# Performance work log

Measured on AMD Instinct MI355X. Metric: run time of the kernel, lower is better.

The kernel has to match this reference:

```python
import jax, jax.numpy as jnp
import numpy as np

EPS = 1e-5
TEMP = 2.0

def _dwconv(x, k, dil):
    # depthwise conv, NCHW, kernel OIHW with I=1, groups=C, 'same' padding
    p = dil
    return jax.lax.conv_general_dilated(
        x, k, window_strides=(1, 1), padding=[(p, p), (p, p)],
        rhs_dilation=(dil, dil),
        dimension_numbers=('NCHW', 'OIHW', 'NCHW'),
        feature_group_count=x.shape[1])

def _bn_gelu(y, g, b, m, v):
    scale = (g / jnp.sqrt(v + EPS))[None, :, None, None]
    z = (y - m[None, :, None, None]) * scale + b[None, :, None, None]
    return jax.nn.gelu(z, approximate=False)  # torch nn.GELU default = exact erf

def _pw(feat, w, b):
    # 1x1 pointwise conv with bias
    return jnp.einsum('oi,bihw->bohw', w, feat) + b[None, :, None, None]

def _forward(x, rw, rb,
             e0_k, e0_g, e0_b, e0_m, e0_v, e0_pw, e0_pb,
             e1_k, e1_g, e1_b, e1_m, e1_v, e1_pw, e1_pb,
             e2_k, e2_g, e2_b, e2_m, e2_v, e2_pw, e2_pb):
    # ---- global routing (eval mode: no noise) ----
    pooled = x.mean(axis=(2, 3))                    # [B, C]
    logits = pooled @ rw.T + rb                     # [B, 3]
    prob = jax.nn.softmax(logits / TEMP, axis=-1)
    tp, ti = jax.lax.top_k(prob, 1)                 # top_k = 1
    w = (tp / tp.sum(axis=-1, keepdims=True))[:, 0] # [B], == 1.0 for k=1
    idx = ti[:, 0]                                  # [B]

    # ---- heterogeneous experts, each over full batch, masked by weight ----
    f0 = _pw(_bn_gelu(_dwconv(x, e0_k, 1), e0_g, e0_b, e0_m, e0_v), e0_pw, e0_pb)
    f1 = _pw(_bn_gelu(_dwconv(x, e1_k, 2), e1_g, e1_b, e1_m, e1_v), e1_pw, e1_pb)
    f2 = _pw(_bn_gelu(jnp.einsum('oi,bihw->bohw', e2_k, x), e2_g, e2_b, e2_m, e2_v), e2_pw, e2_pb)

    out = jnp.zeros_like(x)
    for i, fi in enumerate((f0, f1, f2)):
        wi = jnp.where(idx == i, w, 0.0)[:, None, None, None]
        out = out + wi * fi
    return out

def setup_inputs() -> dict:
    key = jax.random.key(0)
    ks = jax.random.split(key, 24)
    B, C, H, W = 32, 256, 64, 64
    d = {
        'x': jax.random.normal(ks[0], (B, C, H, W), jnp.float32),
        'rw': jax.random.normal(ks[1], (3, C), jnp.float32) * 0.02,
        'rb': jnp.zeros((3,), jnp.float32),
    }
    kshapes = [(C, 1, 3, 3), (C, 1, 3, 3), (C, C)]
    for i in range(3):
        base = 2 + i * 4
        d[f'e{i}_k'] = jax.random.normal(ks[base], kshapes[i], jnp.float32) * 0.1
        d[f'e{i}_g'] = jnp.ones((C,), jnp.float32)
        d[f'e{i}_b'] = jnp.zeros((C,), jnp.float32)
        d[f'e{i}_m'] = jax.random.normal(ks[base + 1], (C,), jnp.float32) * 0.1
        d[f'e{i}_v'] = jax.random.uniform(ks[base + 2], (C,), jnp.float32, 0.5, 1.5)
        d[f'e{i}_pw'] = jax.random.normal(ks[base + 3], (C, C), jnp.float32) / np.sqrt(C)
        d[f'e{i}_pb'] = jnp.zeros((C,), jnp.float32)
    return d

def reference(x, rw, rb,
              e0_k, e0_g, e0_b, e0_m, e0_v, e0_pw, e0_pb,
              e1_k, e1_g, e1_b, e1_m, e1_v, e1_pw, e1_pb,
              e2_k, e2_g, e2_b, e2_m, e2_v, e2_pw, e2_pb):
    return _forward(x, rw, rb,
                    e0_k, e0_g, e0_b, e0_m, e0_v, e0_pw, e0_pb,
                    e1_k, e1_g, e1_b, e1_m, e1_v, e1_pw, e1_pb,
                    e2_k, e2_g, e2_b, e2_m, e2_v, e2_pw, e2_pb)
```

## Files before the change

kernel.cpp:

```cpp
#include <hip/hip_runtime.h>
#include <math.h>

#define C 256
#define H 64
#define W 64
#define B 32
#define HW (H*W)
#define EPS 1e-5f
#define LSTR 72
#define LSTR2 64

typedef __attribute__((ext_vector_type(8))) short short8;
typedef __attribute__((ext_vector_type(4))) short short4v;
typedef __attribute__((ext_vector_type(4))) float f32x4;

__device__ __forceinline__ float gelu_exact(float z) {
    return 0.5f * z * (1.0f + erff(z * 0.70710678f));
}
__device__ __forceinline__ short f2bf(float f) {
    union { float f; unsigned u; } v; v.f = f;
    unsigned r = v.u + 0x7fffu + ((v.u >> 16) & 1u);
    return (short)(r >> 16);
}
__device__ __forceinline__ float bf2f(short s) {
    union { unsigned u; float f; } v; v.u = ((unsigned)(unsigned short)s) << 16;
    return v.f;
}

__global__ __launch_bounds__(256) void pool_kernel(const float* __restrict__ x,
                                                   float* __restrict__ pooled) {
    int bc = blockIdx.x;
    const float4* p4 = (const float4*)(x + (size_t)bc * HW);
    int t = threadIdx.x;
    float s = 0.f;
    for (int i = t; i < HW/4; i += 256) {
        float4 v = p4[i];
        s += v.x + v.y + v.z + v.w;
    }
    for (int off = 32; off > 0; off >>= 1) s += __shfl_down(s, off, 64);
    __shared__ float wsum[4];
    if ((t & 63) == 0) wsum[t >> 6] = s;
    __syncthreads();
    if (t == 0) pooled[bc] = (wsum[0]+wsum[1]+wsum[2]+wsum[3]) * (1.f/HW);
}

__global__ void route_kernel(const float* __restrict__ pooled,
                             const float* __restrict__ rw,
                             const float* __restrict__ rb,
                             int* __restrict__ idx) {
    int b = blockIdx.x;
    int t = threadIdx.x;
    int e = t >> 6, lane = t & 63;
    const float* p = pooled + b*C;
    const float* w = rw + e*C;
    float s = 0.f;
#pragma unroll
    for (int i = 0; i < 4; ++i) s += p[lane + i*64] * w[lane + i*64];
    for (int off = 32; off > 0; off >>= 1) s += __shfl_down(s, off, 64);
    __shared__ float lg[3];
    if (lane == 0) lg[e] = s + rb[e];
    __syncthreads();
    if (t == 0) {
        int best = 0; float bv = lg[0];
        if (lg[1] > bv) { bv = lg[1]; best = 1; }
        if (lg[2] > bv) { bv = lg[2]; best = 2; }
        idx[b] = best;
    }
}

__global__ __launch_bounds__(256) void prep_kernel(
    const float* __restrict__ s0, const float* __restrict__ s1,
    const float* __restrict__ s2, const float* __restrict__ s3,
    const float* __restrict__ e0k, const float* __restrict__ e1k,
    const float* __restrict__ g0, const float* __restrict__ b0,
    const float* __restrict__ m0, const float* __restrict__ v0,
    const float* __restrict__ g1, const float* __restrict__ b1,
    const float* __restrict__ m1, const float* __restrict__ v1,
    const float* __restrict__ g2, const float* __restrict__ b2,
    const float* __restrict__ m2, const float* __restrict__ v2,
    short* __restrict__ apackAll, float* __restrict__ kf0, float* __restrict__ kf1,
    float* __restrict__ scAll, float* __restrict__ shAll)
{
    if (blockIdx.x < 192) {
        int gid = blockIdx.x * 256 + threadIdx.x;
        int mat = gid >> 13;
        int c   = gid & 8191;
        int lane = c & 63;
        int ktmt = c >> 6;
        int mt = ktmt & 15, kt = ktmt >> 4;
        int o  = mt*16 + (lane & 15);
        int ci = kt*32 + (lane >> 4)*8;
        const float* src = (mat == 0) ? s0 : (mat == 1) ? s1 :
                           (mat == 2 || mat == 4) ? s2 : s3;
        bool lo = (mat >= 4);
        const float* p = src + o*C + ci;
        short8 v;
#pragma unroll
        for (int j = 0; j < 8; ++j) {
            float f = p[j];
            short hj = f2bf(f);
            v[j] = lo ? f2bf(f - bf2f(hj)) : hj;
        }
        *(short8*)&apackAll[(size_t)gid * 8] = v;
    } else {
        int t = threadIdx.x;
        {
            float s = g0[t] / sqrtf(v0[t] + EPS);
            scAll[t] = s; shAll[t] = b0[t] - m0[t]*s;
#pragma unroll
            for (int j = 0; j < 9; ++j) kf0[t*12+j] = e0k[t*9+j]*s;
            kf0[t*12+9] = 0.f; kf0[t*12+10] = 0.f; kf0[t*12+11] = 0.f;
        }
        {
            float s = g1[t] / sqrtf(v1[t] + EPS);
            scAll[C+t] = s; shAll[C+t] = b1[t] - m1[t]*s;
#pragma unroll
            for (int j = 0; j < 9; ++j) kf1[t*12+j] = e1k[t*9+j]*s;
            kf1[t*12+9] = 0.f; kf1[t*12+10] = 0.f; kf1[t*12+11] = 0.f;
        }
        {
            float s = g2[t] / sqrtf(v2[t] + EPS);
            scAll[2*C+t] = s; shAll[2*C+t] = b2[t] - m2[t]*s;
        }
    }
}

template<int DIL>
__device__ __forceinline__ void conv_rows(const float* __restrict__ x,
                                          const float* __restrict__ kf,
                                          const float* __restrict__ sh,
                                          short* __restrict__ lds,
                                          int b, int h, int t) {
    const int strip = t & 7;
    const int w0 = strip * 8;
    const int cib = t >> 3;
#pragma unroll 1
    for (int iter = 0; iter < 8; ++iter) {
        int ci = iter*32 + cib;
        const float* xpl = x + (size_t)(b*C + ci) * HW;
        float fr[3][16];
        bool rv[3];
#pragma unroll
        for (int ky = 0; ky < 3; ++ky) {
            int y = h + (ky - 1)*DIL;
            rv[ky] = ((unsigned)y < H);
            if (rv[ky]) {
                const float* row = xpl + y*W;
                float4 fa = (strip > 0) ? *(const float4*)(row + w0 - 4) : float4{0,0,0,0};
                float4 fb = *(const float4*)(row + w0);
                float4 fc = *(const float4*)(row + w0 + 4);
                float4 fd = (strip < 7) ? *(const float4*)(row + w0 + 8) : float4{0,0,0,0};
                fr[ky][0]=fa.x; fr[ky][1]=fa.y; fr[ky][2]=fa.z; fr[ky][3]=fa.w;
                fr[ky][4]=fb.x; fr[ky][5]=fb.y; fr[ky][6]=fb.z; fr[ky][7]=fb.w;
                fr[ky][8]=fc.x; fr[ky][9]=fc.y; fr[ky][10]=fc.z; fr[ky][11]=fc.w;
                fr[ky][12]=fd.x; fr[ky][13]=fd.y; fr[ky][14]=fd.z; fr[ky][15]=fd.w;
            }
        }
        float4 k0 = *(const float4*)(kf + ci*12);
        float4 k1v = *(const float4*)(kf + ci*12 + 4);
        float wk[9] = {k0.x,k0.y,k0.z,k0.w,k1v.x,k1v.y,k1v.z,k1v.w, kf[ci*12+8]};
        float acc8[8] = {0,0,0,0,0,0,0,0};
#pragma unroll
        for (int ky = 0; ky < 3; ++ky) {
            if (rv[ky]) {
#pragma unroll
                for (int kx = 0; kx < 3; ++kx) {
                    float wv = wk[ky*3+kx];
                    const int base = 4 + (kx - 1)*DIL;
#pragma unroll
                    for (int j = 0; j < 8; ++j) acc8[j] += wv * fr[ky][base + j];
                }
            }
        }
        float shv = sh[ci];
        int w0s = w0 ^ ((((unsigned)ci >> 3) & 3) << 4);
        short8 res;
#pragma unroll
        for (int j = 0; j < 8; ++j) res[j] = f2bf(gelu_exact(acc8[j] + shv));
        *(short8*)&lds[ci*LSTR + w0s] = res;
    }
}

__global__ __launch_bounds__(256) void k1_feat(
    const float* __restrict__ x, const int* __restrict__ idx,
    const float* __restrict__ kf0, const float* __restrict__ kf1,
    const float* __restrict__ scAll, const float* __restrict__ shAll,
    short* __restrict__ featfrag)
{
    __shared__ short lds[C*LSTR];
    const int h = blockIdx.x, b = blockIdx.y;
    const int t = threadIdx.x;
    const int lane = t & 63, wid = t >> 6;
    const int l15 = lane & 15, quad = lane >> 4;
    const int e = idx[b];
    if (e >= 2) return;

    if (e == 0) conv_rows<1>(x, kf0, shAll,     lds, b, h, t);
    else        conv_rows<2>(x, kf1, shAll + C, lds, b, h, t);
    __syncthreads();
#pragma unroll
    for (int itr = 0; itr < 8; ++itr) {
        int chunk = itr*4 + wid;
        int kt = chunk & 7, pt = chunk >> 3;
        int wv = pt*16 + l15;
        int cb = kt*32 + quad*8;
        short8 v;
#pragma unroll
        for (int r = 0; r < 8; ++r) {
            int ci = cb + r;
            v[r] = lds[ci*LSTR + (wv ^ ((((unsigned)ci >> 3) & 3) << 4))];
        }
        *(short8*)&featfrag[(((size_t)(b*C + h*4 + pt)*8 + kt)*64 + lane)*8] = v;
    }
}

__device__ __forceinline__ void gemm3(const short* __restrict__ aH,
                                      const short* __restrict__ aL,
                                      const short* __restrict__ ldsA,
                                      const short* __restrict__ ldsB,
                                      int lane, int wid, f32x4 acc[4][4])
{
    const int l15 = lane & 15, quad = lane >> 4;
    for (int kt = 0; kt < 8; ++kt) {
        int cb = kt*32 + quad*8;
        short8 bH[4], bL[4];
#pragma unroll
        for (int wt = 0; wt < 4; ++wt) {
            int wv = (wt*16 + l15) ^ (quad << 4);
            short8 vH, vL;
#pragma unroll
            for (int r = 0; r < 8; ++r) {
                vH[r] = ldsA[(cb + r)*LSTR2 + wv];
                vL[r] = ldsB[(cb + r)*LSTR2 + wv];
            }
            bH[wt] = vH; bL[wt] = vL;
        }
        short8 fH[4], fL[4];
#pragma unroll
        for (int i = 0; i < 4; ++i) {
            size_t off = ((size_t)(kt*16 + wid*4 + i)*64 + lane)*8;
            fH[i] = *(const short8*)&aH[off];
            fL[i] = *(const short8*)&aL[off];
        }
#pragma unroll
        for (int i = 0; i < 4; ++i)
#pragma unroll
            for (int wt = 0; wt < 4; ++wt) {
                acc[i][wt] = __builtin_amdgcn_mfma_f32_16x16x32_bf16(fH[i], bH[wt], acc[i][wt], 0, 0, 0);
                acc[i][wt] = __builtin_amdgcn_mfma_f32_16x16x32_bf16(fH[i], bL[wt], acc[i][wt], 0, 0, 0);
                acc[i][wt] = __builtin_amdgcn_mfma_f32_16x16x32_bf16(fL[i], bH[wt], acc[i][wt], 0, 0, 0);
            }
    }
}

__global__ __launch_bounds__(256) void k1e2(
    const float* __restrict__ x, const int* __restrict__ idx,
    const float* __restrict__ scAll, const float* __restrict__ shAll,
    const short* __restrict__ apackAll, const float* __restrict__ e2pb,
    float* __restrict__ out)
{
    __shared__ short ldsA[C*LSTR2];
    __shared__ short ldsB[C*LSTR2];
    const int h = blockIdx.x, b = blockIdx.y;
    const int t = threadIdx.x;
    const int lane = t & 63, wid = t >> 6;
    const int l15 = lane & 15, quad = lane >> 4;
    if (idx[b] != 2) return;

    {
        const int strip = t & 7, w0 = strip*8, cib = t >> 3;
#pragma unroll 1
        for (int iter = 0; iter < 8; ++iter) {
            int ci = iter*32 + cib;
            const float* row = x + ((size_t)(b*C + ci)*H + h)*W;
            float4 fa = *(const float4*)(row + w0);
            float4 fb = *(const float4*)(row + w0 + 4);
            float f[8] = {fa.x,fa.y,fa.z,fa.w,fb.x,fb.y,fb.z,fb.w};
            short8 hi, lo;
#pragma unroll
            for (int j = 0; j < 8; ++j) {
                short hj = f2bf(f[j]);
                hi[j] = hj;
                lo[j] = f2bf(f[j] - bf2f(hj));
            }
            int w0s = w0 ^ ((((unsigned)ci >> 3) & 3) << 4);
            *(short8*)&ldsA[ci*LSTR2 + w0s] = hi;
            *(short8*)&ldsB[ci*LSTR2 + w0s] = lo;
        }
    }
    __syncthreads();

    f32x4 acc[4][4];
#pragma unroll
    for (int i = 0; i < 4; ++i)
#pragma unroll
        for (int wt = 0; wt < 4; ++wt) acc[i][wt] = (f32x4){0.f,0.f,0.f,0.f};
    gemm3(apackAll + (size_t)3*65536, apackAll + (size_t)5*65536,
          ldsA, ldsB, lane, wid, acc);
    __syncthreads();

    {
        const float* sc2 = scAll + 2*C;
        const float* sh2 = shAll + 2*C;
#pragma unroll
        for (int i = 0; i < 4; ++i) {
            int cob = wid*64 + i*16 + quad*4;
            float4 s4 = *(const float4*)&sc2[cob];
            float4 h4 = *(const float4*)&sh2[cob];
            float ss[4] = {s4.x, s4.y, s4.z, s4.w};
            float hh[4] = {h4.x, h4.y, h4.z, h4.w};
#pragma unroll
            for (int r = 0; r < 4; ++r) {
                int co = cob + r;
                int sw = ((co >> 3) & 3) << 4;
#pragma unroll
                for (int wt = 0; wt < 4; ++wt) {
                    float f = gelu_exact(acc[i][wt][r]*ss[r] + hh[r]);
                    short hj = f2bf(f);
                    short lj = f2bf(f - bf2f(hj));
                    int a = co*LSTR2 + ((wt*16 + l15) ^ sw);
                    ldsA[a] = hj; ldsB[a] = lj;
                }
            }
        }
    }
    __syncthreads();

#pragma unroll
    for (int i = 0; i < 4; ++i)
#pragma unroll
        for (int wt = 0; wt < 4; ++wt) acc[i][wt] = (f32x4){0.f,0.f,0.f,0.f};
    gemm3(apackAll + (size_t)2*65536, apackAll + (size_t)4*65536,
          ldsA, ldsB, lane, wid, acc);

#pragma unroll
    for (int i = 0; i < 4; ++i) {
        int ob = wid*64 + i*16 + quad*4;
        float4 p4 = *(const float4*)&e2pb[ob];
        float pbv[4] = {p4.x, p4.y, p4.z, p4.w};
#pragma unroll
        for (int wt = 0; wt < 4; ++wt) {
            int w = wt*16 + l15;
#pragma unroll
            for (int r = 0; r < 4; ++r) {
                out[((size_t)(b*C + ob + r))*HW + h*W + w] = acc[i][wt][r] + pbv[r];
            }
        }
    }
}

__global__ __launch_bounds__(256) void k2b_out(
    const int* __restrict__ idx, const short* __restrict__ featfrag,
    const short* __restrict__ apackAll,
    const float* __restrict__ e0pb, const float* __restrict__ e1pb,
    float* __restrict__ out)
{
    const int pblk = blockIdx.x;
    const int oblk = blockIdx.y;
    const int b = blockIdx.z;
    const int t = threadIdx.x, lane = t & 63, wid = t >> 6;
    const int l15 = lane & 15, quad = lane >> 4;
    const int e = idx[b];
    if (e >= 2) return;
    const short* pwf = apackAll + (size_t)e * 65536;
    const float* pb = (e == 0) ? e0pb : e1pb;

    f32x4 acc[2][8];
#pragma unroll
    for (int a = 0; a < 2; ++a)
#pragma unroll
        for (int i = 0; i < 8; ++i) acc[a][i] = (f32x4){0.f,0.f,0.f,0.f};

    const short* fbase = featfrag + ((size_t)(b*C + pblk*8 + wid*2)*8)*512;
    for (int kt = 0; kt < 8; ++kt) {
        short8 af[2];
#pragma unroll
        for (int a = 0; a < 2; ++a)
            af[a] = *(const short8*)&fbase[((size_t)(a*8 + kt)*64 + lane)*8];
        short8 bf[8];
#pragma unroll
        for (int i = 0; i < 8; ++i)
            bf[i] = *(const short8*)&pwf[((size_t)(kt*16 + oblk*8 + i)*64 + lane)*8];
#pragma unroll
        for (int a = 0; a < 2; ++a)
#pragma unroll
            for (int i = 0; i < 8; ++i)
                acc[a][i] = __builtin_amdgcn_mfma_f32_16x16x32_bf16(
                    af[a], bf[i], acc[a][i], 0, 0, 0);
    }

#pragma unroll
    for (int i = 0; i < 8; ++i) {
        int o = oblk*128 + i*16 + l15;
        float pbv = pb[o];
#pragma unroll
        for (int a = 0; a < 2; ++a) {
            int p = pblk*128 + wid*32 + a*16 + quad*4;
            f32x4 v = acc[a][i];
            float4 sv = {v[0]+pbv, v[1]+pbv, v[2]+pbv, v[3]+pbv};
            *(float4*)(out + (size_t)(b*C + o)*HW + p) = sv;
        }
    }
}

extern "C" void kernel_launch(void* const* d_in, const int* in_sizes, int n_in,
                              void* d_out, int out_size, void* d_ws, size_t ws_size,
                              hipStream_t stream) {
    const float* x    = (const float*)d_in[0];
    const float* rw   = (const float*)d_in[1];
    const float* rb   = (const float*)d_in[2];
    const float* e0k  = (const float*)d_in[3];
    const float* e0g  = (const float*)d_in[4];
    const float* e0b  = (const float*)d_in[5];
    const float* e0m  = (const float*)d_in[6];
    const float* e0v  = (const float*)d_in[7];
    const float* e0pw = (const float*)d_in[8];
    const float* e0pb = (const float*)d_in[9];
    const float* e1k  = (const float*)d_in[10];
    const float* e1g  = (const float*)d_in[11];
    const float* e1b  = (const float*)d_in[12];
    const float* e1m  = (const float*)d_in[13];
    const float* e1v  = (const float*)d_in[14];
    const float* e1pw = (const float*)d_in[15];
    const float* e1pb = (const float*)d_in[16];
    const float* e2k  = (const float*)d_in[17];
    const float* e2g  = (const float*)d_in[18];
    const float* e2b  = (const float*)d_in[19];
    const float* e2m  = (const float*)d_in[20];
    const float* e2v  = (const float*)d_in[21];
    const float* e2pw = (const float*)d_in[22];
    const float* e2pb = (const float*)d_in[23];
    float* out = (float*)d_out;

    char* wsb = (char*)d_ws;
    float* pooled   = (float*)wsb;
    int*   idx      = (int*)(wsb + 32768);
    float* scAll    = (float*)(wsb + 32896);
    float* shAll    = (float*)(wsb + 35968);
    float* kf0      = (float*)(wsb + 39040);
    float* kf1      = (float*)(wsb + 51328);
    short* apackAll = (short*)(wsb + 63616);
    short* featfrag = (short*)(wsb + (1u << 20));

    pool_kernel<<<B*C, 256, 0, stream>>>(x, pooled);
    route_kernel<<<B, 192, 0, stream>>>(pooled, rw, rb, idx);
    prep_kernel<<<193, 256, 0, stream>>>(e0pw, e1pw, e2pw, e2k, e0k, e1k,
                                         e0g, e0b, e0m, e0v,
                                         e1g, e1b, e1m, e1v,
                                         e2g, e2b, e2m, e2v,
                                         apackAll, kf0, kf1, scAll, shAll);
    k1_feat<<<dim3(H, B), 256, 0, stream>>>(x, idx, kf0, kf1, scAll, shAll,
                                            featfrag);
    k1e2<<<dim3(H, B), 256, 0, stream>>>(x, idx, scAll, shAll, apackAll,
                                         e2pb, out);
    k2b_out<<<dim3(32, 2, B), 256, 0, stream>>>(idx, featfrag, apackAll,
                                                e0pb, e1pb, out);
}
```

Measured before the change: 424.3 us.

## Fuse depthwise conv and pointwise GEMM into one kernel with transposed LDS layout

```diff
diff --git a/kernel.cpp b/kernel.cpp
--- a/kernel.cpp
+++ b/kernel.cpp
@@ -7,8 +7,7 @@
 #define B 32
 #define HW (H*W)
 #define EPS 1e-5f
-#define LSTR 72
-#define LSTR2 64
+#define LSTR2 256
 
 typedef __attribute__((ext_vector_type(8))) short short8;
 typedef __attribute__((ext_vector_type(4))) short short4v;
@@ -25,6 +24,16 @@
 __device__ __forceinline__ float bf2f(short s) {
     union { unsigned u; float f; } v; v.u = ((unsigned)(unsigned short)s) << 16;
     return v.f;
+}
+__device__ __forceinline__ int swz8(int w) {
+    return (((w & 7) ^ ((w >> 3) & 7)) << 3);
+}
+__device__ __forceinline__ void swz_hb(int bx, int by, int& h, int& b) {
+    int wg  = bx + (by << 6);
+    int xcd = wg & 7, lin = wg >> 3;
+    b = lin >> 3;
+    int j = lin & 7;
+    h = (((xcd + b) & 7) << 3) + j;
 }
 
 __global__ __launch_bounds__(256) void pool_kernel(const float* __restrict__ x,
@@ -42,30 +51,6 @@
     if ((t & 63) == 0) wsum[t >> 6] = s;
     __syncthreads();
     if (t == 0) pooled[bc] = (wsum[0]+wsum[1]+wsum[2]+wsum[3]) * (1.f/HW);
-}
-
-__global__ void route_kernel(const float* __restrict__ pooled,
-                             const float* __restrict__ rw,
-                             const float* __restrict__ rb,
-                             int* __restrict__ idx) {
-    int b = blockIdx.x;
-    int t = threadIdx.x;
-    int e = t >> 6, lane = t & 63;
-    const float* p = pooled + b*C;
-    const float* w = rw + e*C;
-    float s = 0.f;
-#pragma unroll
-    for (int i = 0; i < 4; ++i) s += p[lane + i*64] * w[lane + i*64];
-    for (int off = 32; off > 0; off >>= 1) s += __shfl_down(s, off, 64);
-    __shared__ float lg[3];
-    if (lane == 0) lg[e] = s + rb[e];
-    __syncthreads();
-    if (t == 0) {
-        int best = 0; float bv = lg[0];
-        if (lg[1] > bv) { bv = lg[1]; best = 1; }
-        if (lg[2] > bv) { bv = lg[2]; best = 2; }
-        idx[b] = best;
-    }
 }
 
 __global__ __launch_bounds__(256) void prep_kernel(
@@ -78,6 +63,8 @@
     const float* __restrict__ m1, const float* __restrict__ v1,
     const float* __restrict__ g2, const float* __restrict__ b2,
     const float* __restrict__ m2, const float* __restrict__ v2,
+    const float* __restrict__ pooled, const float* __restrict__ rw,
+    const float* __restrict__ rb, int* __restrict__ idx,
     short* __restrict__ apackAll, float* __restrict__ kf0, float* __restrict__ kf1,
     float* __restrict__ scAll, float* __restrict__ shAll)
 {
@@ -102,7 +89,7 @@
             v[j] = lo ? f2bf(f - bf2f(hj)) : hj;
         }
         *(short8*)&apackAll[(size_t)gid * 8] = v;
-    } else {
+    } else if (blockIdx.x == 192) {
         int t = threadIdx.x;
         {
             float s = g0[t] / sqrtf(v0[t] + EPS);
@@ -122,15 +109,40 @@
             float s = g2[t] / sqrtf(v2[t] + EPS);
             scAll[2*C+t] = s; shAll[2*C+t] = b2[t] - m2[t]*s;
         }
+    } else {
+        int t = threadIdx.x;
+        if (t < 192) {
+            int e = t >> 6, lane = t & 63;
+            __shared__ float lg[3*B];
+            for (int b = 0; b < B; ++b) {
+                const float* p = pooled + b*C;
+                const float* w = rw + e*C;
+                float s = 0.f;
+#pragma unroll
+                for (int i = 0; i < 4; ++i) s += p[lane + i*64] * w[lane + i*64];
+                for (int off = 32; off > 0; off >>= 1) s += __shfl_down(s, off, 64);
+                if (lane == 0) lg[b*3 + e] = s + rb[e];
+            }
+            __syncthreads();
+            if (t < B) {
+                float l0 = lg[t*3], l1 = lg[t*3+1], l2 = lg[t*3+2];
+                int best = 0; float bv = l0;
+                if (l1 > bv) { bv = l1; best = 1; }
+                if (l2 > bv) { bv = l2; best = 2; }
+                idx[t] = best;
+            }
+        } else {
+            __syncthreads();
+        }
     }
 }
 
 template<int DIL>
-__device__ __forceinline__ void conv_rows(const float* __restrict__ x,
-                                          const float* __restrict__ kf,
-                                          const float* __restrict__ sh,
-                                          short* __restrict__ lds,
-                                          int b, int h, int t) {
+__device__ __forceinline__ void conv_rows_t(const float* __restrict__ x,
+                                            const float* __restrict__ kf,
+                                            const float* __restrict__ sh,
+                                            short* __restrict__ lds,
+                                            int b, int h, int t) {
     const int strip = t & 7;
     const int w0 = strip * 8;
     const int cib = t >> 3;
@@ -173,67 +185,90 @@
             }
         }
         float shv = sh[ci];
-        int w0s = w0 ^ ((((unsigned)ci >> 3) & 3) << 4);
-        short8 res;
-#pragma unroll
-        for (int j = 0; j < 8; ++j) res[j] = f2bf(gelu_exact(acc8[j] + shv));
-        *(short8*)&lds[ci*LSTR + w0s] = res;
-    }
-}
-
-__global__ __launch_bounds__(256) void k1_feat(
+#pragma unroll
+        for (int j = 0; j < 8; ++j) {
+            int w = w0 + j;
+            lds[w*LSTR2 + (ci ^ swz8(w))] = f2bf(gelu_exact(acc8[j] + shv));
+        }
+    }
+}
+
+__global__ __launch_bounds__(256) void kconv(
     const float* __restrict__ x, const int* __restrict__ idx,
     const float* __restrict__ kf0, const float* __restrict__ kf1,
-    const float* __restrict__ scAll, const float* __restrict__ shAll,
-    short* __restrict__ featfrag)
+    const float* __restrict__ shAll, const short* __restrict__ apackAll,
+    const float* __restrict__ e0pb, const float* __restrict__ e1pb,
+    float* __restrict__ out)
 {
-    __shared__ short lds[C*LSTR];
-    const int h = blockIdx.x, b = blockIdx.y;
+    __shared__ short lds[W*LSTR2];
+    int h, b;
+    swz_hb(blockIdx.x, blockIdx.y, h, b);
+    const int e = idx[b];
+    if (e >= 2) return;
     const int t = threadIdx.x;
     const int lane = t & 63, wid = t >> 6;
     const int l15 = lane & 15, quad = lane >> 4;
-    const int e = idx[b];
-    if (e >= 2) return;
-
-    if (e == 0) conv_rows<1>(x, kf0, shAll,     lds, b, h, t);
-    else        conv_rows<2>(x, kf1, shAll + C, lds, b, h, t);
+
+    if (e == 0) conv_rows_t<1>(x, kf0, shAll,     lds, b, h, t);
+    else        conv_rows_t<2>(x, kf1, shAll + C, lds, b, h, t);
     __syncthreads();
-#pragma unroll
-    for (int itr = 0; itr < 8; ++itr) {
-        int chunk = itr*4 + wid;
-        int kt = chunk & 7, pt = chunk >> 3;
-        int wv = pt*16 + l15;
-        int cb = kt*32 + quad*8;
-        short8 v;
-#pragma unroll
-        for (int r = 0; r < 8; ++r) {
-            int ci = cb + r;
-            v[r] = lds[ci*LSTR + (wv ^ ((((unsigned)ci >> 3) & 3) << 4))];
-        }
-        *(short8*)&featfrag[(((size_t)(b*C + h*4 + pt)*8 + kt)*64 + lane)*8] = v;
-    }
-}
-
-__device__ __forceinline__ void gemm3(const short* __restrict__ aH,
-                                      const short* __restrict__ aL,
-                                      const short* __restrict__ ldsA,
-                                      const short* __restrict__ ldsB,
-                                      int lane, int wid, f32x4 acc[4][4])
+
+    const short* pwf = apackAll + (size_t)e * 65536;
+    f32x4 acc[4][4];
+#pragma unroll
+    for (int i = 0; i < 4; ++i)
+#pragma unroll
+        for (int wt = 0; wt < 4; ++wt) acc[i][wt] = (f32x4){0.f,0.f,0.f,0.f};
+    for (int kt = 0; kt < 8; ++kt) {
+        short8 bf[4];
+#pragma unroll
+        for (int wt = 0; wt < 4; ++wt) {
+            int w = wt*16 + l15;
+            bf[wt] = *(const short8*)&lds[w*LSTR2 + ((kt*32 + quad*8) ^ swz8(w))];
+        }
+        short8 af[4];
+#pragma unroll
+        for (int i = 0; i < 4; ++i)
+            af[i] = *(const short8*)&pwf[((size_t)(kt*16 + wid*4 + i)*64 + lane)*8];
+#pragma unroll
+        for (int i = 0; i < 4; ++i)
+#pragma unroll
+            for (int wt = 0; wt < 4; ++wt)
+                acc[i][wt] = __builtin_amdgcn_mfma_f32_16x16x32_bf16(
+                    af[i], bf[wt], acc[i][wt], 0, 0, 0);
+    }
+
+    const float* pb = (e == 0) ? e0pb : e1pb;
+#pragma unroll
+    for (int i = 0; i < 4; ++i) {
+        int ob = wid*64 + i*16 + quad*4;
+        float4 p4 = *(const float4*)&pb[ob];
+        float pbv[4] = {p4.x, p4.y, p4.z, p4.w};
+#pragma unroll
+        for (int wt = 0; wt < 4; ++wt) {
+            int w = wt*16 + l15;
+#pragma unroll
+            for (int r = 0; r < 4; ++r)
+                out[((size_t)(b*C + ob + r))*HW + h*W + w] = acc[i][wt][r] + pbv[r];
+        }
+    }
+}
+
+__device__ __forceinline__ void gemm3t(const short* __restrict__ aH,
+                                       const short* __restrict__ aL,
+                                       const short* __restrict__ ldsH,
+                                       const short* __restrict__ ldsL,
+                                       int lane, int wid, f32x4 acc[4][4])
 {
     const int l15 = lane & 15, quad = lane >> 4;
     for (int kt = 0; kt < 8; ++kt) {
-        int cb = kt*32 + quad*8;
         short8 bH[4], bL[4];
 #pragma unroll
         for (int wt = 0; wt < 4; ++wt) {
-            int wv = (wt*16 + l15) ^ (quad << 4);
-            short8 vH, vL;
-#pragma unroll
-            for (int r = 0; r < 8; ++r) {
-                vH[r] = ldsA[(cb + r)*LSTR2 + wv];
-                vL[r] = ldsB[(cb + r)*LSTR2 + wv];
-            }
-            bH[wt] = vH; bL[wt] = vL;
+            int w = wt*16 + l15;
+            int off = w*LSTR2 + ((kt*32 + quad*8) ^ swz8(w));
+            bH[wt] = *(const short8*)&ldsH[off];
+            bL[wt] = *(const short8*)&ldsL[off];
         }
         short8 fH[4], fL[4];
 #pragma unroll
@@ -253,29 +288,32 @@
     }
 }
 
-__global__ __launch_bounds__(256) void k1e2(
+__global__ __launch_bounds__(256) void ke2(
     const float* __restrict__ x, const int* __restrict__ idx,
     const float* __restrict__ scAll, const float* __restrict__ shAll,
     const short* __restrict__ apackAll, const float* __restrict__ e2pb,
     float* __restrict__ out)
 {
-    __shared__ short ldsA[C*LSTR2];
-    __shared__ short ldsB[C*LSTR2];
-    const int h = blockIdx.x, b = blockIdx.y;
+    __shared__ short ldsH[W*LSTR2];
+    __shared__ short ldsL[W*LSTR2];
+    int h, b;
+    swz_hb(blockIdx.x, blockIdx.y, h, b);
+    if (idx[b] != 2) return;
     const int t = threadIdx.x;
     const int lane = t & 63, wid = t >> 6;
     const int l15 = lane & 15, quad = lane >> 4;
-    if (idx[b] != 2) return;
 
     {
-        const int strip = t & 7, w0 = strip*8, cib = t >> 3;
+        const int w = t & 63;
+        const int vsw = swz8(w);
+        const int ci0w = wid * 64;
 #pragma unroll 1
-        for (int iter = 0; iter < 8; ++iter) {
-            int ci = iter*32 + cib;
-            const float* row = x + ((size_t)(b*C + ci)*H + h)*W;
-            float4 fa = *(const float4*)(row + w0);
-            float4 fb = *(const float4*)(row + w0 + 4);
-            float f[8] = {fa.x,fa.y,fa.z,fa.w,fb.x,fb.y,fb.z,fb.w};
+        for (int k = 0; k < 8; ++k) {
+            int ci0 = ci0w + k*8;
+            const float* px = x + ((size_t)(b*C + ci0)*H + h)*W + w;
+            float f[8];
+#pragma unroll
+            for (int j = 0; j < 8; ++j) f[j] = px[(size_t)j * HW];
             short8 hi, lo;
 #pragma unroll
             for (int j = 0; j < 8; ++j) {
@@ -283,9 +321,9 @@
                 hi[j] = hj;
                 lo[j] = f2bf(f[j] - bf2f(hj));
             }
-            int w0s = w0 ^ ((((unsigned)ci >> 3) & 3) << 4);
-            *(short8*)&ldsA[ci*LSTR2 + w0s] = hi;
-            *(short8*)&ldsB[ci*LSTR2 + w0s] = lo;
+            int col = ci0 ^ vsw;
+            *(short8*)&ldsH[w*LSTR2 + col] = hi;
+            *(short8*)&ldsL[w*LSTR2 + col] = lo;
         }
     }
     __syncthreads();
@@ -295,8 +333,8 @@
     for (int i = 0; i < 4; ++i)
 #pragma unroll
         for (int wt = 0; wt < 4; ++wt) acc[i][wt] = (f32x4){0.f,0.f,0.f,0.f};
-    gemm3(apackAll + (size_t)3*65536, apackAll + (size_t)5*65536,
-          ldsA, ldsB, lane, wid, acc);
+    gemm3t(apackAll + (size_t)3*65536, apackAll + (size_t)5*65536,
+           ldsH, ldsL, lane, wid, acc);
     __syncthreads();
 
     {
@@ -310,17 +348,19 @@
             float ss[4] = {s4.x, s4.y, s4.z, s4.w};
             float hh[4] = {h4.x, h4.y, h4.z, h4.w};
 #pragma unroll
-            for (int r = 0; r < 4; ++r) {
-                int co = cob + r;
-                int sw = ((co >> 3) & 3) << 4;
-#pragma unroll
-                for (int wt = 0; wt < 4; ++wt) {
+            for (int wt = 0; wt < 4; ++wt) {
+                int w = wt*16 + l15;
+                int col = cob ^ swz8(w);
+                short4v ph, pl;
+#pragma unroll
+                for (int r = 0; r < 4; ++r) {
                     float f = gelu_exact(acc[i][wt][r]*ss[r] + hh[r]);
                     short hj = f2bf(f);
-                    short lj = f2bf(f - bf2f(hj));
-                    int a = co*LSTR2 + ((wt*16 + l15) ^ sw);
-                    ldsA[a] = hj; ldsB[a] = lj;
+                    ph[r] = hj;
+                    pl[r] = f2bf(f - bf2f(hj));
                 }
+                *(short4v*)&ldsH[w*LSTR2 + col] = ph;
+                *(short4v*)&ldsL[w*LSTR2 + col] = pl;
             }
         }
     }
@@ -330,8 +370,8 @@
     for (int i = 0; i < 4; ++i)
 #pragma unroll
         for (int wt = 0; wt < 4; ++wt) acc[i][wt] = (f32x4){0.f,0.f,0.f,0.f};
-    gemm3(apackAll + (size_t)2*65536, apackAll + (size_t)4*65536,
-          ldsA, ldsB, lane, wid, acc);
+    gemm3t(apackAll + (size_t)2*65536, apackAll + (size_t)4*65536,
+           ldsH, ldsL, lane, wid, acc);
 
 #pragma unroll
     for (int i = 0; i < 4; ++i) {
@@ -342,63 +382,8 @@
         for (int wt = 0; wt < 4; ++wt) {
             int w = wt*16 + l15;
 #pragma unroll
-            for (int r = 0; r < 4; ++r) {
+            for (int r = 0; r < 4; ++r)
                 out[((size_t)(b*C + ob + r))*HW + h*W + w] = acc[i][wt][r] + pbv[r];
-            }
-        }
-    }
-}
-
-__global__ __launch_bounds__(256) void k2b_out(
-    const int* __restrict__ idx, const short* __restrict__ featfrag,
-    const short* __restrict__ apackAll,
-    const float* __restrict__ e0pb, const float* __restrict__ e1pb,
-    float* __restrict__ out)
-{
-    const int pblk = blockIdx.x;
-    const int oblk = blockIdx.y;
-    const int b = blockIdx.z;
-    const int t = threadIdx.x, lane = t & 63, wid = t >> 6;
-    const int l15 = lane & 15, quad = lane >> 4;
-    const int e = idx[b];
-    if (e >= 2) return;
-    const short* pwf = apackAll + (size_t)e * 65536;
-    const float* pb = (e == 0) ? e0pb : e1pb;
-
-    f32x4 acc[2][8];
-#pragma unroll
-    for (int a = 0; a < 2; ++a)
-#pragma unroll
-        for (int i = 0; i < 8; ++i) acc[a][i] = (f32x4){0.f,0.f,0.f,0.f};
-
-    const short* fbase = featfrag + ((size_t)(b*C + pblk*8 + wid*2)*8)*512;
-    for (int kt = 0; kt < 8; ++kt) {
-        short8 af[2];
-#pragma unroll
-        for (int a = 0; a < 2; ++a)
-            af[a] = *(const short8*)&fbase[((size_t)(a*8 + kt)*64 + lane)*8];
-        short8 bf[8];
-#pragma unroll
-        for (int i = 0; i < 8; ++i)
-            bf[i] = *(const short8*)&pwf[((size_t)(kt*16 + oblk*8 + i)*64 + lane)*8];
-#pragma unroll
-        for (int a = 0; a < 2; ++a)
-#pragma unroll
-            for (int i = 0; i < 8; ++i)
-                acc[a][i] = __builtin_amdgcn_mfma_f32_16x16x32_bf16(
-                    af[a], bf[i], acc[a][i], 0, 0, 0);
-    }
-
-#pragma unroll
-    for (int i = 0; i < 8; ++i) {
-        int o = oblk*128 + i*16 + l15;
-        float pbv = pb[o];
-#pragma unroll
-        for (int a = 0; a < 2; ++a) {
-            int p = pblk*128 + wid*32 + a*16 + quad*4;
-            f32x4 v = acc[a][i];
-            float4 sv = {v[0]+pbv, v[1]+pbv, v[2]+pbv, v[3]+pbv};
-            *(float4*)(out + (size_t)(b*C + o)*HW + p) = sv;
         }
     }
 }
@@ -440,19 +425,16 @@
     float* kf0      = (float*)(wsb + 39040);
     float* kf1      = (float*)(wsb + 51328);
     short* apackAll = (short*)(wsb + 63616);
-    short* featfrag = (short*)(wsb + (1u << 20));
 
     pool_kernel<<<B*C, 256, 0, stream>>>(x, pooled);
-    route_kernel<<<B, 192, 0, stream>>>(pooled, rw, rb, idx);
-    prep_kernel<<<193, 256, 0, stream>>>(e0pw, e1pw, e2pw, e2k, e0k, e1k,
+    prep_kernel<<<194, 256, 0, stream>>>(e0pw, e1pw, e2pw, e2k, e0k, e1k,
                                          e0g, e0b, e0m, e0v,
                                          e1g, e1b, e1m, e1v,
                                          e2g, e2b, e2m, e2v,
+                                         pooled, rw, rb, idx,
                                          apackAll, kf0, kf1, scAll, shAll);
-    k1_feat<<<dim3(H, B), 256, 0, stream>>>(x, idx, kf0, kf1, scAll, shAll,
-                                            featfrag);
-    k1e2<<<dim3(H, B), 256, 0, stream>>>(x, idx, scAll, shAll, apackAll,
-                                         e2pb, out);
-    k2b_out<<<dim3(32, 2, B), 256, 0, stream>>>(idx, featfrag, apackAll,
-                                                e0pb, e1pb, out);
-}
+    kconv<<<dim3(H, B), 256, 0, stream>>>(x, idx, kf0, kf1, shAll, apackAll,
+                                          e0pb, e1pb, out);
+    ke2<<<dim3(H, B), 256, 0, stream>>>(x, idx, scAll, shAll, apackAll,
+                                        e2pb, out);
+}
```

Result: faster. 407.2 us (-4.0%).
